# Kernel tuning notes

Hardware: AMD Instinct MI355X
Metric: run time of the kernel (lower is better)

Reference implementation:

```python
import jax, jax.numpy as jnp
import numpy as np

N_E = 1024
E_DIM = 64
BETA = 0.25


def setup_inputs() -> dict:
    key = jax.random.key(0)
    k1, k2 = jax.random.split(key)
    z = jax.random.normal(k1, (16, E_DIM, 64, 64), dtype=jnp.float32)
    # embedding initialized uniform(-1/n_e, 1/n_e) as in the torch module
    emb = jax.random.uniform(k2, (N_E, E_DIM), dtype=jnp.float32,
                             minval=-1.0 / N_E, maxval=1.0 / N_E)
    return {"z": z, "emb": emb}


def reference(z, emb):
    n_e, e_dim = emb.shape
    # NCHW -> NHWC, flatten to tokens
    zp = jnp.transpose(z, (0, 2, 3, 1))            # [B,H,W,C]
    zf = zp.reshape(-1, e_dim)                      # [N,C]
    # squared distances ||zf||^2 + ||e||^2 - 2 zf e^T  -> [N, n_e]
    d = (jnp.sum(zf * zf, axis=1, keepdims=True)
         + jnp.sum(emb * emb, axis=1)
         - 2.0 * jnp.matmul(zf, emb.T))
    idx = jnp.argmin(d, axis=1)                     # [N]
    # one-hot @ emb is exactly a gather
    z_q = emb[idx].reshape(zp.shape)                # [B,H,W,C]
    loss = (jnp.mean((jax.lax.stop_gradient(z_q) - zp) ** 2)
            + BETA * jnp.mean((z_q - jax.lax.stop_gradient(zp)) ** 2))
    # straight-through estimator
    z_q = zp + jax.lax.stop_gradient(z_q - zp)
    # perplexity from codeword usage histogram
    counts = jax.ops.segment_sum(jnp.ones_like(idx, dtype=zf.dtype), idx,
                                 num_segments=n_e)
    e_mean = counts / zf.shape[0]
    perplexity = jnp.exp(-jnp.sum(e_mean * jnp.log(e_mean + 1e-10)))
    min_encoding_indices = idx.reshape(z.shape[0], -1).astype(jnp.int32)
    z_q = jnp.transpose(z_q, (0, 3, 1, 2))          # back to NCHW
    return z_q, loss, perplexity, min_encoding_indices
```

## Files before the change

### kernel.cpp

```cpp
#include <hip/hip_runtime.h>

#define TOKS 65536
#define ED 64
#define NE 1024
#define CH_STRIDE 4096
#define B_STRIDE 262144

typedef __bf16 bf16x8 __attribute__((ext_vector_type(8)));
typedef float f32x16 __attribute__((ext_vector_type(16)));
typedef unsigned short ushort_t;
typedef unsigned int uint_t;


__device__ __forceinline__ ushort_t f2bf(float x) {
    uint_t u = __float_as_uint(x);
    uint_t r = u + 0x7FFFu + ((u >> 16) & 1u);
    return (ushort_t)(r >> 16);
}

__global__ __launch_bounds__(256) void vq_prep_e(const float* __restrict__ emb,
                                                 ushort_t* __restrict__ efrag,
                                                 float* __restrict__ enorm,
                                                 int* __restrict__ hist,
                                                 double* __restrict__ lossAcc) {
    const int tid = threadIdx.x;
    const int w = tid >> 6, lane = tid & 63;
    const int j = blockIdx.x * 4 + w;

    const float e = emb[j * 64 + lane];
    const float sq = __fmul_rn(e, e);
    float acc = sq;
    acc = __fadd_rn(acc, __shfl_down(sq, 8, 64));
    acc = __fadd_rn(acc, __shfl_down(sq, 16, 64));
    acc = __fadd_rn(acc, __shfl_down(sq, 24, 64));
    acc = __fadd_rn(acc, __shfl_down(sq, 32, 64));
    acc = __fadd_rn(acc, __shfl_down(sq, 40, 64));
    acc = __fadd_rn(acc, __shfl_down(sq, 48, 64));
    acc = __fadd_rn(acc, __shfl_down(sq, 56, 64));
    float x = __fadd_rn(acc, __shfl_down(acc, 1, 64));
    float y = __fadd_rn(x, __shfl_down(x, 2, 64));
    float zn = __fadd_rn(y, __shfl_down(y, 4, 64));
    if (lane == 0) enorm[j] = zn;

    const ushort_t h = f2bf(-2.0f * e);
    const int ct = j >> 5, m = j & 31;
    const int ks = lane >> 4, kh = (lane >> 3) & 1, i = lane & 7;
    efrag[(size_t)((ct * 4 + ks) * 512) + (m + 32 * kh) * 8 + i] = h;

    if (blockIdx.x < 4) hist[blockIdx.x * 256 + tid] = 0;
    if (blockIdx.x == 0 && tid == 0) *lossAcc = 0.0;
}

__global__ __launch_bounds__(256, 4) void vq_main(
    const float* __restrict__ z,
    const ushort_t* __restrict__ efrag,
    const float* __restrict__ enorm,
    const float* __restrict__ emb,
    float* __restrict__ zq,
    float* __restrict__ out_idx,
    int* __restrict__ hist,
    double* __restrict__ lossAcc) {
    __shared__ float z_s[64][68];
    __shared__ uint_t skey[4][2][32][2][3];
    __shared__ double wsum[4];

    const int tid = threadIdx.x;
    const int w = tid >> 6, lane = tid & 63;
    const int t0 = blockIdx.x * 64;
    const int b = t0 >> 12, hw0 = t0 & 4095;
    const float* zbase = z + (size_t)b * B_STRIDE + hw0;

    {
        const int c = tid >> 2, u0 = (tid & 3) * 16;
        const float4* src = (const float4*)(zbase + (size_t)c * CH_STRIDE + u0);
        float4 f0 = src[0], f1 = src[1], f2 = src[2], f3 = src[3];
        float4* dst = (float4*)&z_s[c][u0];
        dst[0] = f0; dst[1] = f1; dst[2] = f2; dst[3] = f3;
    }
    __syncthreads();

    const int n = lane & 31, kh = lane >> 5;

    bf16x8 zbA[4], zbB[4];
    #pragma unroll
    for (int ks = 0; ks < 4; ++ks) {
        #pragma unroll
        for (int i = 0; i < 8; ++i) {
            const int k = ks * 16 + kh * 8 + i;
            union { ushort_t u; __bf16 bh; } ca, cb;
            ca.u = f2bf(z_s[k][n]);
            cb.u = f2bf(z_s[k][32 + n]);
            zbA[ks][i] = ca.bh;
            zbB[ks][i] = cb.bh;
        }
    }

    uint_t kA0 = 0xFFFFFFFFu, kA1 = 0xFFFFFFFFu, kA2 = 0xFFFFFFFFu;
    uint_t kB0 = 0xFFFFFFFFu, kB1 = 0xFFFFFFFFu, kB2 = 0xFFFFFFFFu;
    const bf16x8* eg = (const bf16x8*)efrag;

    #pragma unroll
    for (int ct = 0; ct < 8; ++ct) {
        const int gct = w * 8 + ct;
        bf16x8 ah[4];
        #pragma unroll
        for (int ks = 0; ks < 4; ++ks)
            ah[ks] = eg[(size_t)(gct * 4 + ks) * 64 + lane];

        const int jb = gct * 32 + 4 * kh;

        f32x16 acc;
        #pragma unroll
        for (int r = 0; r < 16; ++r) acc[r] = 0.25f;
        #pragma unroll
        for (int ks = 0; ks < 4; ++ks)
            acc = __builtin_amdgcn_mfma_f32_32x32x16_bf16(ah[ks], zbA[ks], acc, 0, 0, 0);
        #pragma unroll
        for (int r = 0; r < 16; ++r) {
            uint_t key = (__float_as_uint(acc[r]) & 0xFFFFFC00u)
                         | (uint_t)(jb + (r & 3) + 8 * (r >> 2));
            uint_t mx = max(kA0, key);
            kA2 = min(kA2, max(kA1, mx));
            kA1 = min(kA1, mx);
            kA0 = min(kA0, key);
        }

        #pragma unroll
        for (int r = 0; r < 16; ++r) acc[r] = 0.25f;
        #pragma unroll
        for (int ks = 0; ks < 4; ++ks)
            acc = __builtin_amdgcn_mfma_f32_32x32x16_bf16(ah[ks], zbB[ks], acc, 0, 0, 0);
        #pragma unroll
        for (int r = 0; r < 16; ++r) {
            uint_t key = (__float_as_uint(acc[r]) & 0xFFFFFC00u)
                         | (uint_t)(jb + (r & 3) + 8 * (r >> 2));
            uint_t mx = max(kB0, key);
            kB2 = min(kB2, max(kB1, mx));
            kB1 = min(kB1, mx);
            kB0 = min(kB0, key);
        }
    }

    skey[w][0][n][kh][0] = kA0; skey[w][0][n][kh][1] = kA1; skey[w][0][n][kh][2] = kA2;
    skey[w][1][n][kh][0] = kB0; skey[w][1][n][kh][1] = kB1; skey[w][1][n][kh][2] = kB2;
    __syncthreads();

    const int t_loc = tid >> 2, cw = tid & 3;
    const int tile = t_loc >> 5, nn = t_loc & 31;
    uint_t ck[6];
    #pragma unroll
    for (int hi = 0; hi < 2; ++hi)
        #pragma unroll
        for (int s = 0; s < 3; ++s)
            ck[hi * 3 + s] = skey[cw][tile][nn][hi][s];

    uint_t kmin = ck[0];
    #pragma unroll
    for (int c2 = 1; c2 < 6; ++c2) kmin = min(kmin, ck[c2]);
    kmin = min(kmin, (uint_t)__shfl_xor((int)kmin, 1, 64));
    kmin = min(kmin, (uint_t)__shfl_xor((int)kmin, 2, 64));
    const float thr = __uint_as_float(kmin & 0xFFFFFC00u) + 4.0e-4f;

    float rr[8];
    #pragma unroll
    for (int m = 0; m < 8; ++m) {
        float a = z_s[m][t_loc];
        rr[m] = __fmul_rn(a, a);
    }
    #pragma unroll
    for (int i = 8; i < 64; i += 8) {
        #pragma unroll
        for (int m = 0; m < 8; ++m) {
            float a = z_s[i + m][t_loc];
            rr[m] = __fadd_rn(rr[m], __fmul_rn(a, a));
        }
    }
    const float zn =
        __fadd_rn(__fadd_rn(__fadd_rn(rr[0], rr[1]), __fadd_rn(rr[2], rr[3])),
                  __fadd_rn(__fadd_rn(rr[4], rr[5]), __fadd_rn(rr[6], rr[7])));

    float bd = 3.4e38f; int bj = 1 << 30;
    #pragma unroll
    for (int c2 = 0; c2 < 6; ++c2) {
        const float vc = __uint_as_float(ck[c2] & 0xFFFFFC00u);
        if (vc <= thr) {
            const int j = (int)(ck[c2] & 1023u);
            const float* e = emb + (size_t)j * 64;
            float a0 = 0.f;
            #pragma unroll
            for (int k4 = 0; k4 < 64; k4 += 4) {
                float4 e4 = *(const float4*)(e + k4);
                a0 = __fmaf_rn(z_s[k4 + 0][t_loc], e4.x, a0);
                a0 = __fmaf_rn(z_s[k4 + 1][t_loc], e4.y, a0);
                a0 = __fmaf_rn(z_s[k4 + 2][t_loc], e4.z, a0);
                a0 = __fmaf_rn(z_s[k4 + 3][t_loc], e4.w, a0);
            }
            float d = __fsub_rn(__fadd_rn(zn, enorm[j]), 2.0f * a0);
            if (d < bd || (d == bd && j < bj)) { bd = d; bj = j; }
        }
    }
    {
        float pd = __shfl_xor(bd, 1, 64); int pj = __shfl_xor(bj, 1, 64);
        if (pd < bd || (pd == bd && pj < bj)) { bd = pd; bj = pj; }
        pd = __shfl_xor(bd, 2, 64); pj = __shfl_xor(bj, 2, 64);
        if (pd < bd || (pd == bd && pj < bj)) { bd = pd; bj = pj; }
    }

    double ls = 0.0;
    if (cw == 0) {
        out_idx[t0 + t_loc] = (float)bj;
        atomicAdd(&hist[bj], 1);
        const float* e = emb + (size_t)bj * 64;
        #pragma unroll
        for (int k = 0; k < 64; ++k) {
            float ev = e[k];
            float zv = z_s[k][t_loc];
            z_s[k][t_loc] = ev;
            float df = ev - zv;
            ls += (double)(df * df);
        }
    }
    #pragma unroll
    for (int off = 32; off > 0; off >>= 1) ls += __shfl_down(ls, off, 64);
    if (lane == 0) wsum[w] = ls;
    __syncthreads();
    if (tid == 0)
        atomicAdd(lossAcc, wsum[0] + wsum[1] + wsum[2] + wsum[3]);

    {
        const int c = tid >> 2, u0 = (tid & 3) * 16;
        const float4* s4 = (const float4*)&z_s[c][u0];
        float4 f0 = s4[0], f1 = s4[1], f2 = s4[2], f3 = s4[3];
        float4* dst = (float4*)(zq + (size_t)b * B_STRIDE + (size_t)c * CH_STRIDE + hw0 + u0);
        dst[0] = f0; dst[1] = f1; dst[2] = f2; dst[3] = f3;
    }
}

__global__ __launch_bounds__(256) void vq_final(const int* __restrict__ hist,
                                                const double* __restrict__ lossAcc,
                                                float* __restrict__ outs) {
    __shared__ double red[256];
    double acc = 0.0;
    for (int j = threadIdx.x; j < NE; j += 256) {
        double em = (double)hist[j] * (1.0 / 65536.0);
        acc += em * log(em + 1e-10);
    }
    red[threadIdx.x] = acc;
    __syncthreads();
    for (int s = 128; s > 0; s >>= 1) {
        if (threadIdx.x < s) red[threadIdx.x] += red[threadIdx.x + s];
        __syncthreads();
    }
    if (threadIdx.x == 0) {
        outs[0] = (float)(1.25 * (*lossAcc) * (1.0 / 4194304.0));
        outs[1] = (float)exp(-red[0]);
    }
}

extern "C" void kernel_launch(void* const* d_in, const int* in_sizes, int n_in,
                              void* d_out, int out_size, void* d_ws, size_t ws_size,
                              hipStream_t stream) {
    const float* z = (const float*)d_in[0];
    const float* emb = (const float*)d_in[1];
    float* out = (float*)d_out;

    char* ws = (char*)d_ws;
    ushort_t* efrag = (ushort_t*)ws;
    float* enorm = (float*)(ws + 131072);
    int* hist = (int*)(ws + 135168);
    double* lossAcc = (double*)(ws + 139264);

    float* zq = out;
    float* scalars = out + 4194304;
    float* out_idx = out + 4194306;

    vq_prep_e<<<256, 256, 0, stream>>>(emb, efrag, enorm, hist, lossAcc);
    vq_main<<<1024, 256, 0, stream>>>(z, efrag, enorm, emb, zq, out_idx, hist, lossAcc);
    vq_final<<<1, 256, 0, stream>>>(hist, lossAcc, scalars);
}
```

Before: 49.64 us.

## Halve tokens per block to cut registers and double occupancy in VQ kernel

After: 101.5 us. 104% more time.

```diff
diff --git a/kernel.cpp b/kernel.cpp
--- a/kernel.cpp
+++ b/kernel.cpp
@@ -51,7 +51,7 @@
     if (blockIdx.x == 0 && tid == 0) *lossAcc = 0.0;
 }
 
-__global__ __launch_bounds__(256, 4) void vq_main(
+__global__ __launch_bounds__(256, 8) void vq_main(
     const float* __restrict__ z,
     const ushort_t* __restrict__ efrag,
     const float* __restrict__ enorm,
@@ -60,105 +60,82 @@
     float* __restrict__ out_idx,
     int* __restrict__ hist,
     double* __restrict__ lossAcc) {
-    __shared__ float z_s[64][68];
-    __shared__ uint_t skey[4][2][32][2][3];
+    __shared__ float z_s[64][36];
+    __shared__ uint_t skey[4][32][2][3];
     __shared__ double wsum[4];
 
     const int tid = threadIdx.x;
     const int w = tid >> 6, lane = tid & 63;
-    const int t0 = blockIdx.x * 64;
+    const int t0 = blockIdx.x * 32;
     const int b = t0 >> 12, hw0 = t0 & 4095;
     const float* zbase = z + (size_t)b * B_STRIDE + hw0;
 
     {
-        const int c = tid >> 2, u0 = (tid & 3) * 16;
-        const float4* src = (const float4*)(zbase + (size_t)c * CH_STRIDE + u0);
-        float4 f0 = src[0], f1 = src[1], f2 = src[2], f3 = src[3];
-        float4* dst = (float4*)&z_s[c][u0];
-        dst[0] = f0; dst[1] = f1; dst[2] = f2; dst[3] = f3;
+        const int c = tid >> 2, u0 = (tid & 3) * 8;
+        const float* src = zbase + (size_t)c * CH_STRIDE + u0;
+        float4 f0 = *(const float4*)(src);
+        float4 f1 = *(const float4*)(src + 4);
+        *(float4*)&z_s[c][u0] = f0;
+        *(float4*)&z_s[c][u0 + 4] = f1;
     }
     __syncthreads();
 
     const int n = lane & 31, kh = lane >> 5;
 
-    bf16x8 zbA[4], zbB[4];
+    bf16x8 zb[4];
     #pragma unroll
     for (int ks = 0; ks < 4; ++ks) {
         #pragma unroll
         for (int i = 0; i < 8; ++i) {
-            const int k = ks * 16 + kh * 8 + i;
-            union { ushort_t u; __bf16 bh; } ca, cb;
-            ca.u = f2bf(z_s[k][n]);
-            cb.u = f2bf(z_s[k][32 + n]);
-            zbA[ks][i] = ca.bh;
-            zbB[ks][i] = cb.bh;
-        }
-    }
-
-    uint_t kA0 = 0xFFFFFFFFu, kA1 = 0xFFFFFFFFu, kA2 = 0xFFFFFFFFu;
-    uint_t kB0 = 0xFFFFFFFFu, kB1 = 0xFFFFFFFFu, kB2 = 0xFFFFFFFFu;
+            union { ushort_t u; __bf16 bh; } ca;
+            ca.u = f2bf(z_s[ks * 16 + kh * 8 + i][n]);
+            zb[ks][i] = ca.bh;
+        }
+    }
+
+    uint_t k0 = 0xFFFFFFFFu, k1 = 0xFFFFFFFFu, k2 = 0xFFFFFFFFu;
     const bf16x8* eg = (const bf16x8*)efrag;
 
     #pragma unroll
     for (int ct = 0; ct < 8; ++ct) {
         const int gct = w * 8 + ct;
-        bf16x8 ah[4];
-        #pragma unroll
-        for (int ks = 0; ks < 4; ++ks)
-            ah[ks] = eg[(size_t)(gct * 4 + ks) * 64 + lane];
+        bf16x8 ah0 = eg[(size_t)(gct * 4 + 0) * 64 + lane];
+        bf16x8 ah1 = eg[(size_t)(gct * 4 + 1) * 64 + lane];
+        bf16x8 ah2 = eg[(size_t)(gct * 4 + 2) * 64 + lane];
+        bf16x8 ah3 = eg[(size_t)(gct * 4 + 3) * 64 + lane];
+
+        f32x16 acc;
+        #pragma unroll
+        for (int r = 0; r < 16; ++r) acc[r] = 0.25f;
+        acc = __builtin_amdgcn_mfma_f32_32x32x16_bf16(ah0, zb[0], acc, 0, 0, 0);
+        acc = __builtin_amdgcn_mfma_f32_32x32x16_bf16(ah1, zb[1], acc, 0, 0, 0);
+        acc = __builtin_amdgcn_mfma_f32_32x32x16_bf16(ah2, zb[2], acc, 0, 0, 0);
+        acc = __builtin_amdgcn_mfma_f32_32x32x16_bf16(ah3, zb[3], acc, 0, 0, 0);
 
         const int jb = gct * 32 + 4 * kh;
-
-        f32x16 acc;
-        #pragma unroll
-        for (int r = 0; r < 16; ++r) acc[r] = 0.25f;
-        #pragma unroll
-        for (int ks = 0; ks < 4; ++ks)
-            acc = __builtin_amdgcn_mfma_f32_32x32x16_bf16(ah[ks], zbA[ks], acc, 0, 0, 0);
         #pragma unroll
         for (int r = 0; r < 16; ++r) {
             uint_t key = (__float_as_uint(acc[r]) & 0xFFFFFC00u)
                          | (uint_t)(jb + (r & 3) + 8 * (r >> 2));
-            uint_t mx = max(kA0, key);
-            kA2 = min(kA2, max(kA1, mx));
-            kA1 = min(kA1, mx);
-            kA0 = min(kA0, key);
-        }
-
-        #pragma unroll
-        for (int r = 0; r < 16; ++r) acc[r] = 0.25f;
-        #pragma unroll
-        for (int ks = 0; ks < 4; ++ks)
-            acc = __builtin_amdgcn_mfma_f32_32x32x16_bf16(ah[ks], zbB[ks], acc, 0, 0, 0);
-        #pragma unroll
-        for (int r = 0; r < 16; ++r) {
-            uint_t key = (__float_as_uint(acc[r]) & 0xFFFFFC00u)
-                         | (uint_t)(jb + (r & 3) + 8 * (r >> 2));
-            uint_t mx = max(kB0, key);
-            kB2 = min(kB2, max(kB1, mx));
-            kB1 = min(kB1, mx);
-            kB0 = min(kB0, key);
-        }
-    }
-
-    skey[w][0][n][kh][0] = kA0; skey[w][0][n][kh][1] = kA1; skey[w][0][n][kh][2] = kA2;
-    skey[w][1][n][kh][0] = kB0; skey[w][1][n][kh][1] = kB1; skey[w][1][n][kh][2] = kB2;
-    __syncthreads();
-
-    const int t_loc = tid >> 2, cw = tid & 3;
-    const int tile = t_loc >> 5, nn = t_loc & 31;
-    uint_t ck[6];
-    #pragma unroll
-    for (int hi = 0; hi < 2; ++hi)
-        #pragma unroll
-        for (int s = 0; s < 3; ++s)
-            ck[hi * 3 + s] = skey[cw][tile][nn][hi][s];
-
-    uint_t kmin = ck[0];
-    #pragma unroll
-    for (int c2 = 1; c2 < 6; ++c2) kmin = min(kmin, ck[c2]);
+            uint_t mx = max(k0, key);
+            k2 = min(k2, max(k1, mx));
+            k1 = min(k1, mx);
+            k0 = min(k0, key);
+        }
+    }
+
+    skey[w][n][kh][0] = k0; skey[w][n][kh][1] = k1; skey[w][n][kh][2] = k2;
+    __syncthreads();
+
+    const int t_loc = tid >> 3, cw = tid & 7;
+    uint_t ck[3];
+    #pragma unroll
+    for (int s = 0; s < 3; ++s) ck[s] = skey[cw >> 1][t_loc][cw & 1][s];
+
+    uint_t kmin = min(ck[0], min(ck[1], ck[2]));
     kmin = min(kmin, (uint_t)__shfl_xor((int)kmin, 1, 64));
     kmin = min(kmin, (uint_t)__shfl_xor((int)kmin, 2, 64));
+    kmin = min(kmin, (uint_t)__shfl_xor((int)kmin, 4, 64));
     const float thr = __uint_as_float(kmin & 0xFFFFFC00u) + 4.0e-4f;
 
     float rr[8];
@@ -181,7 +158,7 @@
 
     float bd = 3.4e38f; int bj = 1 << 30;
     #pragma unroll
-    for (int c2 = 0; c2 < 6; ++c2) {
+    for (int c2 = 0; c2 < 3; ++c2) {
         const float vc = __uint_as_float(ck[c2] & 0xFFFFFC00u);
         if (vc <= thr) {
             const int j = (int)(ck[c2] & 1023u);
@@ -199,24 +176,30 @@
             if (d < bd || (d == bd && j < bj)) { bd = d; bj = j; }
         }
     }
-    {
-        float pd = __shfl_xor(bd, 1, 64); int pj = __shfl_xor(bj, 1, 64);
+    #pragma unroll
+    for (int m = 1; m < 8; m <<= 1) {
+        float pd = __shfl_xor(bd, m, 64);
+        int pj = __shfl_xor(bj, m, 64);
         if (pd < bd || (pd == bd && pj < bj)) { bd = pd; bj = pj; }
-        pd = __shfl_xor(bd, 2, 64); pj = __shfl_xor(bj, 2, 64);
-        if (pd < bd || (pd == bd && pj < bj)) { bd = pd; bj = pj; }
-    }
-
-    double ls = 0.0;
+    }
+
     if (cw == 0) {
         out_idx[t0 + t_loc] = (float)bj;
         atomicAdd(&hist[bj], 1);
-        const float* e = emb + (size_t)bj * 64;
-        #pragma unroll
-        for (int k = 0; k < 64; ++k) {
-            float ev = e[k];
+    }
+
+    double ls = 0.0;
+    {
+        const float* e = emb + (size_t)bj * 64 + cw * 8;
+        float4 ea = *(const float4*)(e);
+        float4 eb = *(const float4*)(e + 4);
+        float ev[8] = {ea.x, ea.y, ea.z, ea.w, eb.x, eb.y, eb.z, eb.w};
+        #pragma unroll
+        for (int i = 0; i < 8; ++i) {
+            const int k = cw * 8 + i;
             float zv = z_s[k][t_loc];
-            z_s[k][t_loc] = ev;
-            float df = ev - zv;
+            z_s[k][t_loc] = ev[i];
+            float df = ev[i] - zv;
             ls += (double)(df * df);
         }
     }
@@ -228,11 +211,12 @@
         atomicAdd(lossAcc, wsum[0] + wsum[1] + wsum[2] + wsum[3]);
 
     {
-        const int c = tid >> 2, u0 = (tid & 3) * 16;
-        const float4* s4 = (const float4*)&z_s[c][u0];
-        float4 f0 = s4[0], f1 = s4[1], f2 = s4[2], f3 = s4[3];
-        float4* dst = (float4*)(zq + (size_t)b * B_STRIDE + (size_t)c * CH_STRIDE + hw0 + u0);
-        dst[0] = f0; dst[1] = f1; dst[2] = f2; dst[3] = f3;
+        const int c = tid >> 2, u0 = (tid & 3) * 8;
+        float4 f0 = *(const float4*)&z_s[c][u0];
+        float4 f1 = *(const float4*)&z_s[c][u0 + 4];
+        float* dst = zq + (size_t)b * B_STRIDE + (size_t)c * CH_STRIDE + hw0 + u0;
+        *(float4*)(dst) = f0;
+        *(float4*)(dst + 4) = f1;
     }
 }
 
@@ -275,6 +259,6 @@
     float* out_idx = out + 4194306;
 
     vq_prep_e<<<256, 256, 0, stream>>>(emb, efrag, enorm, hist, lossAcc);
-    vq_main<<<1024, 256, 0, stream>>>(z, efrag, enorm, emb, zq, out_idx, hist, lossAcc);
+    vq_main<<<2048, 256, 0, stream>>>(z, efrag, enorm, emb, zq, out_idx, hist, lossAcc);
     vq_final<<<1, 256, 0, stream>>>(hist, lossAcc, scalars);
 }
```
